# Kernel optimization log

Measured on AMD Instinct MI355X. Metric: run time of the kernel, lower is better.

Reference implementation:

```python
import jax, jax.numpy as jnp
import numpy as np

N = 20000      # nodes
E = 640000     # edges (avg degree 32)
IN = 32        # input_dim
HID = 256      # hidden_dim
H = 8          # num_heads
Dh = HID // H  # head_dim = 32
TD = 32        # time_dim
L = 3          # num_layers
OUT = 2


def setup_inputs() -> dict:
    key = jax.random.key(0)
    ks = jax.random.split(key, 20)
    def w(k, sh):
        return (jax.random.normal(k, sh, jnp.float32) * 0.05)
    return {
        "x": jax.random.normal(ks[0], (N, IN), jnp.float32),
        "timestamps": jax.random.uniform(ks[1], (N,), jnp.float32),
        "edge_index": jax.random.randint(ks[2], (2, E), 0, N, jnp.int32),
        "batch": jnp.zeros((N,), jnp.int32),
        "time_freq": jax.random.normal(ks[3], (TD // 2,), jnp.float32),
        "inW": w(ks[4], (IN, HID)), "inb": jnp.zeros((HID,), jnp.float32),
        "qW": w(ks[5], (L, HID + TD, HID)), "qb": jnp.zeros((L, HID), jnp.float32),
        "kW": w(ks[6], (L, HID + TD, HID)), "kb": jnp.zeros((L, HID), jnp.float32),
        "vW": w(ks[7], (L, HID, HID)), "vb": jnp.zeros((L, HID), jnp.float32),
        "oW": w(ks[8], (L, HID, HID)), "ob": jnp.zeros((L, HID), jnp.float32),
        "c1W": w(ks[9], (HID, HID // 2)), "c1b": jnp.zeros((HID // 2,), jnp.float32),
        "c2W": w(ks[10], (HID // 2, OUT)), "c2b": jnp.zeros((OUT,), jnp.float32),
    }


def reference(x, timestamps, time_freq, inW, inb, qW, qb, kW, kb, vW, vb,
              oW, ob, c1W, c1b, c2W, c2b, edge_index, batch):
    n = x.shape[0]
    src, dst = edge_index[0], edge_index[1]

    # Functional time encoding (node-level timestamps branch)
    t = (timestamps - timestamps.min()) / (timestamps.max() - timestamps.min() + 1e-8)
    wt = t[:, None] * time_freq[None, :]                      # [N, TD/2]
    tf = jnp.concatenate([jnp.cos(wt), jnp.sin(wt)], axis=-1)  # [N, TD]

    h = x @ inW + inb                                          # [N, HID]
    scale = 1.0 / np.sqrt(Dh).astype(np.float32)

    for l in range(L):
        xt = jnp.concatenate([h, tf], axis=-1)                 # [N, HID+TD]
        Q = (xt @ qW[l] + qb[l]).reshape(n, H, Dh)
        K = (xt @ kW[l] + kb[l]).reshape(n, H, Dh)
        V = (h @ vW[l] + vb[l]).reshape(n, H, Dh)

        # per-edge attention scores [E, H]
        scores = jnp.einsum('ehd,ehd->eh', Q[dst], K[src]) * scale

        # segment softmax over incoming edges of each dst node
        m = jax.ops.segment_max(scores, dst, num_segments=n)   # [N, H]
        e = jnp.exp(scores - m[dst])
        s = jax.ops.segment_sum(e, dst, num_segments=n)        # [N, H]
        att = e / s[dst]                                       # [E, H]

        msgs = att[..., None] * V[src]                         # [E, H, Dh]
        out = jax.ops.segment_sum(msgs, dst, num_segments=n)   # [N, H, Dh]
        out = out.reshape(n, HID) @ oW[l] + ob[l]
        h = jax.nn.elu(out)

    # global mean pool (single graph: batch all zeros)
    cnt = jax.ops.segment_sum(jnp.ones((n, 1), h.dtype), batch, num_segments=1)
    g = jax.ops.segment_sum(h, batch, num_segments=1) / jnp.maximum(cnt, 1.0)

    logits = jax.nn.relu(g @ c1W + c1b) @ c2W + c2b            # [1, OUT]
    return logits
```

## Files before the change

### kernel.cpp

```cpp
#include <hip/hip_runtime.h>
#include <math.h>

#define HID 256
#define TD 32
#define NL 3
#define C1DIM 128
#define OUTDIM 2
#define QKVW 768

using half8  = __attribute__((ext_vector_type(8))) _Float16;
using half4v = __attribute__((ext_vector_type(4))) _Float16;
using half2v = __attribute__((ext_vector_type(2))) _Float16;
using f32x4  = __attribute__((ext_vector_type(4))) float;

typedef __attribute__((address_space(1))) void gbl_void_t;
typedef __attribute__((address_space(3))) void lds_void_t;

__device__ __forceinline__ void load16_to_lds(const void* g, void* l) {
  __builtin_amdgcn_global_load_lds((const gbl_void_t*)g, (lds_void_t*)l, 16, 0, 0);
}

__device__ __forceinline__ float dot8h(half8 a, half8 b, float acc) {
#if __has_builtin(__builtin_amdgcn_fdot2)
  union { half8 v; half2v h2[4]; } ua, ub;
  ua.v = a; ub.v = b;
#pragma unroll
  for (int j = 0; j < 4; ++j) acc = __builtin_amdgcn_fdot2(ua.h2[j], ub.h2[j], acc, false);
  return acc;
#else
#pragma unroll
  for (int j = 0; j < 8; ++j) acc += (float)a[j] * (float)b[j];
  return acc;
#endif
}

__global__ __launch_bounds__(1024) void k_tsmm(const float* __restrict__ ts,
                                               float* __restrict__ mmf,
                                               int* __restrict__ deg, int n) {
  int t = threadIdx.x;
  float lmin = INFINITY, lmax = -INFINITY;
  for (int i = t; i < n; i += 1024) {
    float v = ts[i];
    lmin = fminf(lmin, v);
    lmax = fmaxf(lmax, v);
    deg[i] = 0;
  }
#pragma unroll
  for (int off = 32; off >= 1; off >>= 1) {
    lmin = fminf(lmin, __shfl_xor(lmin, off));
    lmax = fmaxf(lmax, __shfl_xor(lmax, off));
  }
  __shared__ float wmin[16], wmax[16];
  int lane = t & 63, w = t >> 6;
  if (lane == 0) { wmin[w] = lmin; wmax[w] = lmax; }
  __syncthreads();
  if (t == 0) {
    float a = INFINITY, b = -INFINITY;
    for (int i = 0; i < 16; ++i) { a = fminf(a, wmin[i]); b = fmaxf(b, wmax[i]); }
    mmf[0] = a; mmf[1] = b;
  }
}

__global__ void k_enc(const float* __restrict__ ts, const float* __restrict__ freq,
                      const float* __restrict__ mmf, const float* __restrict__ x,
                      _Float16* __restrict__ tfh, _Float16* __restrict__ xh, int n) {
  int idx = blockIdx.x * blockDim.x + threadIdx.x;
  int nt = n * TD;
  if (idx < nt) {
    int node = idx >> 5, j = idx & 31;
    float t = (ts[node] - mmf[0]) / (mmf[1] - mmf[0] + 1e-8f);
    float w = t * freq[j & 15];
    tfh[idx] = (_Float16)((j < 16) ? cosf(w) : sinf(w));
  } else if (idx < nt + n * 32) {
    int i2 = idx - nt;
    xh[i2] = (_Float16)x[i2];
  }
}

__global__ void k_prep(const float* __restrict__ inW, const float* __restrict__ qW,
                       const float* __restrict__ kW, const float* __restrict__ vW,
                       const float* __restrict__ oW, const float* __restrict__ qb,
                       const float* __restrict__ kb, const float* __restrict__ vb,
                       _Float16* __restrict__ inWt, _Float16* __restrict__ qkvWt,
                       float* __restrict__ qkvb, _Float16* __restrict__ oWt) {
  int idx = blockIdx.x * blockDim.x + threadIdx.x;
  const int S0 = 32 * HID;
  const int KQ = HID + TD;
  const int S1 = NL * QKVW * KQ;
  const int S2 = NL * QKVW;
  const int S3 = NL * HID * HID;
  if (idx < S0) {
    int nrow = idx / 32, k = idx - nrow * 32;
    inWt[idx] = (_Float16)inW[k * HID + nrow];
  } else if ((idx -= S0) < S1) {
    int l = idx / (QKVW * KQ);
    int rem = idx - l * (QKVW * KQ);
    int nrow = rem / KQ;
    int k = rem - nrow * KQ;
    float v;
    if (nrow < 256)      v = qW[(size_t)l * KQ * HID + (size_t)k * HID + nrow];
    else if (nrow < 512) v = kW[(size_t)l * KQ * HID + (size_t)k * HID + (nrow - 256)];
    else                 v = (k < HID) ? vW[(size_t)l * HID * HID + (size_t)k * HID + (nrow - 512)] : 0.f;
    qkvWt[idx] = (_Float16)v;
  } else if ((idx -= S1) < S2) {
    int l = idx / QKVW;
    int j = idx - l * QKVW;
    float v;
    if (j < 256)      v = qb[l * HID + j];
    else if (j < 512) v = kb[l * HID + (j - 256)];
    else              v = vb[l * HID + (j - 512)];
    qkvb[idx] = v;
  } else if ((idx -= S2) < S3) {
    int l = idx / (HID * HID);
    int rem = idx - l * (HID * HID);
    int nrow = rem / HID;
    int k = rem - nrow * HID;
    oWt[idx] = (_Float16)oW[(size_t)l * HID * HID + (size_t)k * HID + nrow];
  }
}

__global__ void k_count(const int* __restrict__ dst, int* deg, int e) {
  int i = blockIdx.x * blockDim.x + threadIdx.x;
  if (i < e) atomicAdd(&deg[dst[i]], 1);
}

__global__ __launch_bounds__(256) void k_scan_part(const int* __restrict__ deg,
                                                   int* __restrict__ bsum, int n) {
  int t = threadIdx.x;
  int idx = blockIdx.x * 256 + t;
  int v = (idx < n) ? deg[idx] : 0;
  int lane = t & 63, w = t >> 6;
  int x = v;
#pragma unroll
  for (int off = 1; off < 64; off <<= 1) {
    int y = __shfl_up(x, off);
    if (lane >= off) x += y;
  }
  __shared__ int ws[4];
  if (lane == 63) ws[w] = x;
  __syncthreads();
  if (t == 0) bsum[blockIdx.x] = ws[0] + ws[1] + ws[2] + ws[3];
}

__global__ __launch_bounds__(64) void k_scan_mid(const int* __restrict__ bsum,
                                                 int* __restrict__ boff, int nb) {
  int lane = threadIdx.x;
  int carry = 0;
  for (int base = 0; base < nb; base += 64) {
    int i = base + lane;
    int v = (i < nb) ? bsum[i] : 0;
    int x = v;
#pragma unroll
    for (int off = 1; off < 64; off <<= 1) {
      int y = __shfl_up(x, off);
      if (lane >= off) x += y;
    }
    if (i < nb) boff[i] = carry + x - v;
    carry += __shfl(x, 63);
  }
}

__global__ __launch_bounds__(256) void k_scan_apply(const int* __restrict__ deg,
                                                    const int* __restrict__ boff,
                                                    int* __restrict__ row_ptr,
                                                    int* __restrict__ cursor, int n, int e) {
  int t = threadIdx.x;
  int idx = blockIdx.x * 256 + t;
  int v = (idx < n) ? deg[idx] : 0;
  int lane = t & 63, w = t >> 6;
  int x = v;
#pragma unroll
  for (int off = 1; off < 64; off <<= 1) {
    int y = __shfl_up(x, off);
    if (lane >= off) x += y;
  }
  __shared__ int ws[4];
  if (lane == 63) ws[w] = x;
  __syncthreads();
  int wpre = 0;
  for (int i = 0; i < w; ++i) wpre += ws[i];
  if (idx < n) {
    row_ptr[idx] = boff[blockIdx.x] + wpre + x - v;
    cursor[idx] = 0;
  }
  if (idx == 0) row_ptr[n] = e;
}

__global__ void k_scatter(const int* __restrict__ src, const int* __restrict__ dst,
                          const int* __restrict__ row_ptr, int* cursor,
                          int* __restrict__ colbuf, int e) {
  int i = blockIdx.x * blockDim.x + threadIdx.x;
  if (i >= e) return;
  int d = dst[i];
  int p = atomicAdd(&cursor[d], 1);
  colbuf[row_ptr[d] + p] = src[i];
}

__global__ __launch_bounds__(256) void k_gemm_f16(
    const _Float16* __restrict__ A1, int K1,
    const _Float16* __restrict__ A2, int K2,
    const _Float16* __restrict__ Bt,
    const float* __restrict__ bias,
    _Float16* __restrict__ C,
    _Float16* __restrict__ Qb,
    _Float16* __restrict__ KV,
    int M, int Ncols, int Ktot, int mode) {
  __shared__ half8 smem8[2 * 768];
  char* smem = (char*)smem8;
  const int tid = threadIdx.x;
  const int lane = tid & 63, wave = tid >> 6;
  const int wm = wave >> 1, wn = wave & 1;
  const int row0 = blockIdx.y * 128;
  const int col0 = blockIdx.x * 64;

  auto stage = [&](int buf, int k0) {
    char* sA = smem + buf * 12288;
    char* sB = sA + 8192;
#pragma unroll
    for (int i = 0; i < 2; ++i) {
      int kg = i * 2 + (wave >> 1);
      int row = (wave & 1) * 64 + lane;
      int grow = row0 + row; if (grow > M - 1) grow = M - 1;
      int k = k0 + kg * 8;
      const _Float16* src = (k < K1) ? (A1 + (size_t)grow * K1 + k)
                                     : (A2 + (size_t)grow * K2 + (k - K1));
      load16_to_lds(src, sA + (i * 256 + wave * 64) * 16);
    }
    {
      const _Float16* src = Bt + (size_t)(col0 + lane) * Ktot + k0 + wave * 8;
      load16_to_lds(src, sB + wave * 64 * 16);
    }
  };

  f32x4 acc[4][2];
#pragma unroll
  for (int mf = 0; mf < 4; ++mf)
#pragma unroll
    for (int nf = 0; nf < 2; ++nf) acc[mf][nf] = f32x4{0.f, 0.f, 0.f, 0.f};

  const int nsteps = Ktot >> 5;
  int cur = 0;
  stage(0, 0);
  __syncthreads();
  for (int st = 0; st < nsteps; ++st) {
    if (st + 1 < nsteps) stage(cur ^ 1, (st + 1) * 32);
    char* sA = smem + cur * 12288;
    char* sB = sA + 8192;
    half8 af[4], bf[2];
#pragma unroll
    for (int mf = 0; mf < 4; ++mf) {
      int slot = (lane >> 4) * 128 + wm * 64 + mf * 16 + (lane & 15);
      af[mf] = *(const half8*)(sA + slot * 16);
    }
#pragma unroll
    for (int nf = 0; nf < 2; ++nf) {
      int slot = (lane >> 4) * 64 + wn * 32 + nf * 16 + (lane & 15);
      bf[nf] = *(const half8*)(sB + slot * 16);
    }
#pragma unroll
    for (int mf = 0; mf < 4; ++mf)
#pragma unroll
      for (int nf = 0; nf < 2; ++nf)
        acc[mf][nf] = __builtin_amdgcn_mfma_f32_16x16x32_f16(af[mf], bf[nf], acc[mf][nf], 0, 0, 0);
    __syncthreads();
    cur ^= 1;
  }

  const int rbase = row0 + wm * 64 + (lane >> 4) * 4;
  const int cbase = col0 + wn * 32 + (lane & 15);
#pragma unroll
  for (int nf = 0; nf < 2; ++nf) {
    int col = cbase + nf * 16;
    float bv = bias[col];
    if (mode != 2) {
#pragma unroll
      for (int mf = 0; mf < 4; ++mf) {
#pragma unroll
        for (int r = 0; r < 4; ++r) {
          int row = rbase + mf * 16 + r;
          if (row < M) {
            float v = acc[mf][nf][r] + bv;
            if (mode == 1) v = (v > 0.f) ? v : expm1f(v);
            C[(size_t)row * Ncols + col] = (_Float16)v;
          }
        }
      }
    } else {
      bool isQ = col < 256;
      int cc = col - 256;
      int isV = cc >> 8;
      int c2 = cc & 255;
      int hh = c2 >> 5, dim = c2 & 31;
      size_t kvoff = ((size_t)hh * M) * 64 + isV * 32 + dim;
#pragma unroll
      for (int mf = 0; mf < 4; ++mf) {
#pragma unroll
        for (int r = 0; r < 4; ++r) {
          int row = rbase + mf * 16 + r;
          if (row < M) {
            float v = acc[mf][nf][r] + bv;
            if (isQ) Qb[(size_t)row * HID + col] = (_Float16)v;
            else     KV[kvoff + (size_t)row * 64] = (_Float16)v;
          }
        }
      }
    }
  }
}

__global__ __launch_bounds__(256) void k_attn(const _Float16* __restrict__ Qb,
                                              const _Float16* __restrict__ KV,
                                              const int* __restrict__ row_ptr,
                                              const int* __restrict__ colbuf,
                                              _Float16* __restrict__ out, int n) {
  int h = blockIdx.x & 7;
  int node = (blockIdx.x >> 3) * 64 + (threadIdx.x >> 2);
  if (node >= n) return;
  int j = threadIdx.x & 3;
  const float scale = 0.17677669529663687f;
  const _Float16* KVh = KV + ((size_t)h * n) * 64;

  half8 qh = *(const half8*)(Qb + (size_t)node * HID + h * 32 + j * 8);
  half8 qs;
#pragma unroll
  for (int q = 0; q < 8; ++q) qs[q] = (_Float16)((float)qh[q] * scale);

  int beg = row_ptr[node], end = row_ptr[node + 1];
  float m = -INFINITY, s = 0.f;
  float a[8] = {0.f, 0.f, 0.f, 0.f, 0.f, 0.f, 0.f, 0.f};

  for (int i = beg; i < end; i += 4) {
    half8 kk[4], vv[4];
#pragma unroll
    for (int t = 0; t < 4; ++t) {
      int ii = i + t; if (ii > end - 1) ii = end - 1;
      int sn = colbuf[ii];
      const _Float16* b = KVh + ((size_t)sn) * 64 + j * 8;
      kk[t] = *(const half8*)(b);
      vv[t] = *(const half8*)(b + 32);
    }
    float p[4];
#pragma unroll
    for (int t = 0; t < 4; ++t) p[t] = dot8h(qs, kk[t], 0.f);
#pragma unroll
    for (int t = 0; t < 4; ++t) {
      p[t] += __shfl_xor(p[t], 1);
      p[t] += __shfl_xor(p[t], 2);
      if (i + t >= end) p[t] = -INFINITY;
    }
#pragma unroll
    for (int t = 0; t < 4; ++t) {
      float sc_ = p[t];
      if (sc_ <= m) {
        float e2 = __expf(sc_ - m);
        s += e2;
#pragma unroll
        for (int q = 0; q < 8; ++q) a[q] = fmaf(e2, (float)vv[t][q], a[q]);
      } else {
        float f = __expf(m - sc_);
        s = s * f + 1.f;
#pragma unroll
        for (int q = 0; q < 8; ++q) a[q] = fmaf(a[q], f, (float)vv[t][q]);
        m = sc_;
      }
    }
  }

  float inv = (s > 0.f) ? (1.f / s) : 0.f;
  half8 o;
#pragma unroll
  for (int q = 0; q < 8; ++q) o[q] = (_Float16)(a[q] * inv);
  *(half8*)(out + (size_t)node * HID + h * 32 + j * 8) = o;
}

__global__ __launch_bounds__(256) void k_pool_partial(const _Float16* __restrict__ h,
                                                      float* __restrict__ partial, int n) {
  int b = blockIdx.x, t = threadIdx.x;
  float s = 0.f;
  for (int r = b; r < n; r += 256) s += (float)h[(size_t)r * HID + t];
  partial[b * HID + t] = s;
}

__global__ __launch_bounds__(256) void k_final(const float* __restrict__ partial,
                                               const float* __restrict__ c1W,
                                               const float* __restrict__ c1b,
                                               const float* __restrict__ c2W,
                                               const float* __restrict__ c2b,
                                               float* __restrict__ out, int n) {
  __shared__ float gl[HID];
  __shared__ float r1[C1DIM];
  int t = threadIdx.x;
  float s = 0.f;
  for (int b = 0; b < 256; b++) s += partial[b * HID + t];
  gl[t] = s / (float)n;
  __syncthreads();
  if (t < C1DIM) {
    float a = c1b[t];
    for (int k = 0; k < HID; k++) a += gl[k] * c1W[k * C1DIM + t];
    r1[t] = fmaxf(a, 0.f);
  }
  __syncthreads();
  if (t < OUTDIM) {
    float a = c2b[t];
    for (int k = 0; k < C1DIM; k++) a += r1[k] * c2W[k * OUTDIM + t];
    out[t] = a;
  }
}

extern "C" void kernel_launch(void* const* d_in, const int* in_sizes, int n_in,
                              void* d_out, int out_size, void* d_ws, size_t ws_size,
                              hipStream_t stream) {
  const float* x    = (const float*)d_in[0];
  const float* ts   = (const float*)d_in[1];
  const int*   ei   = (const int*)d_in[2];
  const float* freq = (const float*)d_in[4];
  const float* inW  = (const float*)d_in[5];
  const float* inb  = (const float*)d_in[6];
  const float* qW   = (const float*)d_in[7];
  const float* qb   = (const float*)d_in[8];
  const float* kW   = (const float*)d_in[9];
  const float* kb   = (const float*)d_in[10];
  const float* vW   = (const float*)d_in[11];
  const float* vb   = (const float*)d_in[12];
  const float* oW   = (const float*)d_in[13];
  const float* ob   = (const float*)d_in[14];
  const float* c1W  = (const float*)d_in[15];
  const float* c1b  = (const float*)d_in[16];
  const float* c2W  = (const float*)d_in[17];
  const float* c2b  = (const float*)d_in[18];

  int n = in_sizes[1];
  int e = in_sizes[2] / 2;
  const int* src = ei;
  const int* dst = ei + e;
  int nb = (n + 255) / 256;

  char* w = (char*)d_ws;
  size_t off = 0;
  auto alloc = [&](size_t bytes) -> char* {
    char* p = w + off;
    off = (off + bytes + 255) & ~(size_t)255;
    return p;
  };
  _Float16* tfh     = (_Float16*)alloc((size_t)n * TD * 2);
  _Float16* xh      = (_Float16*)alloc((size_t)n * 32 * 2);
  _Float16* h       = (_Float16*)alloc((size_t)n * HID * 2);
  _Float16* Qbuf    = (_Float16*)alloc((size_t)n * HID * 2);
  _Float16* KV      = (_Float16*)alloc((size_t)n * 512 * 2);
  _Float16* ao      = (_Float16*)alloc((size_t)n * HID * 2);
  _Float16* inWt    = (_Float16*)alloc((size_t)32 * HID * 2);
  _Float16* qkvWt   = (_Float16*)alloc((size_t)NL * QKVW * (HID + TD) * 2);
  float*    qkvb    = (float*)alloc((size_t)NL * QKVW * 4);
  _Float16* oWt     = (_Float16*)alloc((size_t)NL * HID * HID * 2);
  int*      deg     = (int*)alloc((size_t)n * 4);
  int*      cursor  = (int*)alloc((size_t)n * 4);
  int*      row_ptr = (int*)alloc((size_t)(n + 1) * 4);
  int*      colbuf  = (int*)alloc((size_t)e * 4);
  int*      bsum    = (int*)alloc((size_t)nb * 4);
  int*      boff    = (int*)alloc((size_t)nb * 4);
  float*    partial = (float*)alloc((size_t)256 * HID * 4);
  float*    mmf     = (float*)alloc(256);

  int b256 = 256;
  hipLaunchKernelGGL(k_tsmm, dim3(1), dim3(1024), 0, stream, ts, mmf, deg, n);
  hipLaunchKernelGGL(k_enc, dim3((n * 64 + 255) / 256), dim3(b256), 0, stream,
                     ts, freq, mmf, x, tfh, xh, n);
  {
    int total = 32 * HID + NL * QKVW * (HID + TD) + NL * QKVW + NL * HID * HID;
    hipLaunchKernelGGL(k_prep, dim3((total + 255) / 256), dim3(b256), 0, stream,
                       inW, qW, kW, vW, oW, qb, kb, vb, inWt, qkvWt, qkvb, oWt);
  }
  hipLaunchKernelGGL(k_count, dim3((e + 255) / 256), dim3(b256), 0, stream, dst, deg, e);
  hipLaunchKernelGGL(k_scan_part, dim3(nb), dim3(b256), 0, stream, deg, bsum, n);
  hipLaunchKernelGGL(k_scan_mid, dim3(1), dim3(64), 0, stream, bsum, boff, nb);
  hipLaunchKernelGGL(k_scan_apply, dim3(nb), dim3(b256), 0, stream, deg, boff, row_ptr, cursor, n, e);
  hipLaunchKernelGGL(k_scatter, dim3((e + 255) / 256), dim3(b256), 0, stream, src, dst, row_ptr, cursor, colbuf, e);

  dim3 ggrid_h(HID / 64, (n + 127) / 128);
  dim3 ggrid_qkv(QKVW / 64, (n + 127) / 128);
  hipLaunchKernelGGL(k_gemm_f16, ggrid_h, dim3(b256), 0, stream,
                     xh, 32, xh, 32, inWt, inb, h, (_Float16*)nullptr, (_Float16*)nullptr,
                     n, HID, 32, 0);

  int nchunks = (n + 63) / 64;
  for (int l = 0; l < NL; ++l) {
    const _Float16* qkvWtl = qkvWt + (size_t)l * QKVW * (HID + TD);
    const float*    qkvbl  = qkvb + (size_t)l * QKVW;
    const _Float16* oWtl   = oWt + (size_t)l * HID * HID;
    hipLaunchKernelGGL(k_gemm_f16, ggrid_qkv, dim3(b256), 0, stream,
                       h, HID, tfh, TD, qkvWtl, qkvbl, (_Float16*)nullptr, Qbuf, KV,
                       n, QKVW, HID + TD, 2);
    hipLaunchKernelGGL(k_attn, dim3(nchunks * 8), dim3(b256), 0, stream,
                       Qbuf, KV, row_ptr, colbuf, ao, n);
    hipLaunchKernelGGL(k_gemm_f16, ggrid_h, dim3(b256), 0, stream,
                       ao, HID, ao, HID, oWtl, ob + l * HID, h, (_Float16*)nullptr, (_Float16*)nullptr,
                       n, HID, HID, 1);
  }

  hipLaunchKernelGGL(k_pool_partial, dim3(256), dim3(b256), 0, stream, h, partial, n);
  hipLaunchKernelGGL(k_final, dim3(1), dim3(b256), 0, stream, partial, c1W, c1b, c2W, c2b, (float*)d_out, n);
}
```

Baseline: 481.1 us.

## Fuse setup kernels and widen QKV GEMM tile to 128x128

```diff
diff --git a/kernel.cpp b/kernel.cpp
--- a/kernel.cpp
+++ b/kernel.cpp
@@ -9,7 +9,6 @@
 #define QKVW 768
 
 using half8  = __attribute__((ext_vector_type(8))) _Float16;
-using half4v = __attribute__((ext_vector_type(4))) _Float16;
 using half2v = __attribute__((ext_vector_type(2))) _Float16;
 using f32x4  = __attribute__((ext_vector_type(4))) float;
 
@@ -34,88 +33,147 @@
 #endif
 }
 
-__global__ __launch_bounds__(1024) void k_tsmm(const float* __restrict__ ts,
-                                               float* __restrict__ mmf,
-                                               int* __restrict__ deg, int n) {
+#define NB_ENC 512
+#define NB_QKV (NL * 9 * 12)
+#define NB_O   (NL * 8 * 4)
+#define NB_IN  4
+#define NB_B   9
+
+__global__ __launch_bounds__(256) void k_setup(
+    const float* __restrict__ ts, const float* __restrict__ freq,
+    const float* __restrict__ x,
+    const float* __restrict__ inW, const float* __restrict__ qW,
+    const float* __restrict__ kW, const float* __restrict__ vW,
+    const float* __restrict__ oW, const float* __restrict__ qb,
+    const float* __restrict__ kb, const float* __restrict__ vb,
+    _Float16* __restrict__ tfh, _Float16* __restrict__ xh,
+    _Float16* __restrict__ inWt, _Float16* __restrict__ qkvWt,
+    float* __restrict__ qkvb, _Float16* __restrict__ oWt, int n) {
+  __shared__ _Float16 lds[32][65];
+  int bid = blockIdx.x;
   int t = threadIdx.x;
-  float lmin = INFINITY, lmax = -INFINITY;
-  for (int i = t; i < n; i += 1024) {
-    float v = ts[i];
-    lmin = fminf(lmin, v);
-    lmax = fmaxf(lmax, v);
-    deg[i] = 0;
-  }
-#pragma unroll
-  for (int off = 32; off >= 1; off >>= 1) {
-    lmin = fminf(lmin, __shfl_xor(lmin, off));
-    lmax = fmaxf(lmax, __shfl_xor(lmax, off));
-  }
-  __shared__ float wmin[16], wmax[16];
-  int lane = t & 63, w = t >> 6;
-  if (lane == 0) { wmin[w] = lmin; wmax[w] = lmax; }
-  __syncthreads();
-  if (t == 0) {
-    float a = INFINITY, b = -INFINITY;
-    for (int i = 0; i < 16; ++i) { a = fminf(a, wmin[i]); b = fmaxf(b, wmax[i]); }
-    mmf[0] = a; mmf[1] = b;
-  }
-}
-
-__global__ void k_enc(const float* __restrict__ ts, const float* __restrict__ freq,
-                      const float* __restrict__ mmf, const float* __restrict__ x,
-                      _Float16* __restrict__ tfh, _Float16* __restrict__ xh, int n) {
-  int idx = blockIdx.x * blockDim.x + threadIdx.x;
-  int nt = n * TD;
-  if (idx < nt) {
-    int node = idx >> 5, j = idx & 31;
-    float t = (ts[node] - mmf[0]) / (mmf[1] - mmf[0] + 1e-8f);
-    float w = t * freq[j & 15];
-    tfh[idx] = (_Float16)((j < 16) ? cosf(w) : sinf(w));
-  } else if (idx < nt + n * 32) {
-    int i2 = idx - nt;
-    xh[i2] = (_Float16)x[i2];
-  }
-}
-
-__global__ void k_prep(const float* __restrict__ inW, const float* __restrict__ qW,
-                       const float* __restrict__ kW, const float* __restrict__ vW,
-                       const float* __restrict__ oW, const float* __restrict__ qb,
-                       const float* __restrict__ kb, const float* __restrict__ vb,
-                       _Float16* __restrict__ inWt, _Float16* __restrict__ qkvWt,
-                       float* __restrict__ qkvb, _Float16* __restrict__ oWt) {
-  int idx = blockIdx.x * blockDim.x + threadIdx.x;
-  const int S0 = 32 * HID;
   const int KQ = HID + TD;
-  const int S1 = NL * QKVW * KQ;
-  const int S2 = NL * QKVW;
-  const int S3 = NL * HID * HID;
-  if (idx < S0) {
-    int nrow = idx / 32, k = idx - nrow * 32;
-    inWt[idx] = (_Float16)inW[k * HID + nrow];
-  } else if ((idx -= S0) < S1) {
-    int l = idx / (QKVW * KQ);
-    int rem = idx - l * (QKVW * KQ);
-    int nrow = rem / KQ;
-    int k = rem - nrow * KQ;
-    float v;
-    if (nrow < 256)      v = qW[(size_t)l * KQ * HID + (size_t)k * HID + nrow];
-    else if (nrow < 512) v = kW[(size_t)l * KQ * HID + (size_t)k * HID + (nrow - 256)];
-    else                 v = (k < HID) ? vW[(size_t)l * HID * HID + (size_t)k * HID + (nrow - 512)] : 0.f;
-    qkvWt[idx] = (_Float16)v;
-  } else if ((idx -= S1) < S2) {
-    int l = idx / QKVW;
-    int j = idx - l * QKVW;
-    float v;
-    if (j < 256)      v = qb[l * HID + j];
-    else if (j < 512) v = kb[l * HID + (j - 256)];
-    else              v = vb[l * HID + (j - 512)];
-    qkvb[idx] = v;
-  } else if ((idx -= S2) < S3) {
-    int l = idx / (HID * HID);
-    int rem = idx - l * (HID * HID);
-    int nrow = rem / HID;
-    int k = rem - nrow * HID;
-    oWt[idx] = (_Float16)oW[(size_t)l * HID * HID + (size_t)k * HID + nrow];
+
+  if (bid < NB_ENC) {
+    float lmin = INFINITY, lmax = -INFINITY;
+    for (int i = t; i < n; i += 256) {
+      float v = ts[i];
+      lmin = fminf(lmin, v); lmax = fmaxf(lmax, v);
+    }
+#pragma unroll
+    for (int off = 32; off >= 1; off >>= 1) {
+      lmin = fminf(lmin, __shfl_xor(lmin, off));
+      lmax = fmaxf(lmax, __shfl_xor(lmax, off));
+    }
+    __shared__ float wmin[4], wmax[4];
+    int lane = t & 63, w = t >> 6;
+    if (lane == 0) { wmin[w] = lmin; wmax[w] = lmax; }
+    __syncthreads();
+    float tmin = fminf(fminf(wmin[0], wmin[1]), fminf(wmin[2], wmin[3]));
+    float tmax = fmaxf(fmaxf(wmax[0], wmax[1]), fmaxf(wmax[2], wmax[3]));
+    float inv = 1.f / (tmax - tmin + 1e-8f);
+    int nt = n * TD;
+    int total = n * 64;
+    for (int idx = bid * 256 + t; idx < total; idx += NB_ENC * 256) {
+      if (idx < nt) {
+        int node = idx >> 5, j = idx & 31;
+        float tv = (ts[node] - tmin) * inv;
+        float wv = tv * freq[j & 15];
+        tfh[idx] = (_Float16)((j < 16) ? cosf(wv) : sinf(wv));
+      } else {
+        int i2 = idx - nt;
+        xh[i2] = (_Float16)x[i2];
+      }
+    }
+    return;
+  }
+  bid -= NB_ENC;
+
+  if (bid < NB_QKV) {
+    int l = bid / 108;
+    int rem = bid - l * 108;
+    int kt = rem / 12, ntile = rem - kt * 12;
+    int k0 = kt * 32, n0 = ntile * 64;
+#pragma unroll
+    for (int it = 0; it < 8; ++it) {
+      int i = it * 256 + t;
+      int kk = i >> 6, nn = i & 63;
+      int k = k0 + kk, nrow = n0 + nn;
+      float v;
+      if (nrow < 256)      v = qW[(size_t)l * KQ * HID + (size_t)k * HID + nrow];
+      else if (nrow < 512) v = kW[(size_t)l * KQ * HID + (size_t)k * HID + (nrow - 256)];
+      else                 v = (k < HID) ? vW[(size_t)l * HID * HID + (size_t)k * HID + (nrow - 512)] : 0.f;
+      lds[kk][nn] = (_Float16)v;
+    }
+    __syncthreads();
+    {
+      int nn = t >> 2, kq = (t & 3) * 8;
+      _Float16* dst = qkvWt + (size_t)l * QKVW * KQ + (size_t)(n0 + nn) * KQ + k0 + kq;
+      half8 v;
+#pragma unroll
+      for (int j = 0; j < 8; ++j) v[j] = lds[kq + j][nn];
+      *(half8*)dst = v;
+    }
+    return;
+  }
+  bid -= NB_QKV;
+
+  if (bid < NB_O) {
+    int l = bid / 32;
+    int rem = bid - l * 32;
+    int kt = rem / 4, ntile = rem - kt * 4;
+    int k0 = kt * 32, n0 = ntile * 64;
+#pragma unroll
+    for (int it = 0; it < 8; ++it) {
+      int i = it * 256 + t;
+      int kk = i >> 6, nn = i & 63;
+      lds[kk][nn] = (_Float16)oW[(size_t)l * HID * HID + (size_t)(k0 + kk) * HID + n0 + nn];
+    }
+    __syncthreads();
+    {
+      int nn = t >> 2, kq = (t & 3) * 8;
+      _Float16* dst = oWt + (size_t)l * HID * HID + (size_t)(n0 + nn) * HID + k0 + kq;
+      half8 v;
+#pragma unroll
+      for (int j = 0; j < 8; ++j) v[j] = lds[kq + j][nn];
+      *(half8*)dst = v;
+    }
+    return;
+  }
+  bid -= NB_O;
+
+  if (bid < NB_IN) {
+    int n0 = bid * 64;
+#pragma unroll
+    for (int it = 0; it < 8; ++it) {
+      int i = it * 256 + t;
+      int kk = i >> 6, nn = i & 63;
+      lds[kk][nn] = (_Float16)inW[(size_t)kk * HID + n0 + nn];
+    }
+    __syncthreads();
+    {
+      int nn = t >> 2, kq = (t & 3) * 8;
+      _Float16* dst = inWt + (size_t)(n0 + nn) * 32 + kq;
+      half8 v;
+#pragma unroll
+      for (int j = 0; j < 8; ++j) v[j] = lds[kq + j][nn];
+      *(half8*)dst = v;
+    }
+    return;
+  }
+  bid -= NB_IN;
+
+  {
+    int idx = bid * 256 + t;
+    if (idx < NL * QKVW) {
+      int l = idx / QKVW;
+      int j = idx - l * QKVW;
+      float v;
+      if (j < 256)      v = qb[l * HID + j];
+      else if (j < 512) v = kb[l * HID + (j - 256)];
+      else              v = vb[l * HID + (j - 512)];
+      qkvb[idx] = v;
+    }
   }
 }
 
@@ -202,8 +260,6 @@
     const _Float16* __restrict__ Bt,
     const float* __restrict__ bias,
     _Float16* __restrict__ C,
-    _Float16* __restrict__ Qb,
-    _Float16* __restrict__ KV,
     int M, int Ncols, int Ktot, int mode) {
   __shared__ half8 smem8[2 * 768];
   char* smem = (char*)smem8;
@@ -272,36 +328,112 @@
   for (int nf = 0; nf < 2; ++nf) {
     int col = cbase + nf * 16;
     float bv = bias[col];
-    if (mode != 2) {
-#pragma unroll
-      for (int mf = 0; mf < 4; ++mf) {
-#pragma unroll
-        for (int r = 0; r < 4; ++r) {
-          int row = rbase + mf * 16 + r;
-          if (row < M) {
-            float v = acc[mf][nf][r] + bv;
-            if (mode == 1) v = (v > 0.f) ? v : expm1f(v);
-            C[(size_t)row * Ncols + col] = (_Float16)v;
-          }
+#pragma unroll
+    for (int mf = 0; mf < 4; ++mf) {
+#pragma unroll
+      for (int r = 0; r < 4; ++r) {
+        int row = rbase + mf * 16 + r;
+        if (row < M) {
+          float v = acc[mf][nf][r] + bv;
+          if (mode == 1) v = (v > 0.f) ? v : expm1f(v);
+          C[(size_t)row * Ncols + col] = (_Float16)v;
         }
       }
-    } else {
-      bool isQ = col < 256;
-      int cc = col - 256;
-      int isV = cc >> 8;
-      int c2 = cc & 255;
-      int hh = c2 >> 5, dim = c2 & 31;
-      size_t kvoff = ((size_t)hh * M) * 64 + isV * 32 + dim;
-#pragma unroll
-      for (int mf = 0; mf < 4; ++mf) {
-#pragma unroll
-        for (int r = 0; r < 4; ++r) {
-          int row = rbase + mf * 16 + r;
-          if (row < M) {
-            float v = acc[mf][nf][r] + bv;
-            if (isQ) Qb[(size_t)row * HID + col] = (_Float16)v;
-            else     KV[kvoff + (size_t)row * 64] = (_Float16)v;
-          }
+    }
+  }
+}
+
+__global__ __launch_bounds__(256) void k_gemm_qkv(
+    const _Float16* __restrict__ A1, int K1,
+    const _Float16* __restrict__ A2, int K2,
+    const _Float16* __restrict__ Bt,
+    const float* __restrict__ bias,
+    _Float16* __restrict__ Qb,
+    _Float16* __restrict__ KV,
+    int M, int Ktot) {
+  __shared__ half8 smem8[2048];
+  char* smem = (char*)smem8;
+  const int tid = threadIdx.x;
+  const int lane = tid & 63, wave = tid >> 6;
+  const int wm = wave >> 1, wn = wave & 1;
+  const int row0 = blockIdx.y * 128;
+  const int col0 = blockIdx.x * 128;
+
+  auto stage = [&](int buf, int k0) {
+    char* sA = smem + buf * 16384;
+    char* sB = sA + 8192;
+    int k = k0 + wave * 8;
+#pragma unroll
+    for (int j = 0; j < 2; ++j) {
+      int row = j * 64 + lane;
+      int grow = row0 + row; if (grow > M - 1) grow = M - 1;
+      const _Float16* srcA = (k < K1) ? (A1 + (size_t)grow * K1 + k)
+                                      : (A2 + (size_t)grow * K2 + (k - K1));
+      load16_to_lds(srcA, sA + (wave * 128 + j * 64) * 16);
+    }
+#pragma unroll
+    for (int j = 0; j < 2; ++j) {
+      int col = j * 64 + lane;
+      const _Float16* srcB = Bt + (size_t)(col0 + col) * Ktot + k;
+      load16_to_lds(srcB, sB + (wave * 128 + j * 64) * 16);
+    }
+  };
+
+  f32x4 acc[4][4];
+#pragma unroll
+  for (int mf = 0; mf < 4; ++mf)
+#pragma unroll
+    for (int nf = 0; nf < 4; ++nf) acc[mf][nf] = f32x4{0.f, 0.f, 0.f, 0.f};
+
+  const int nsteps = Ktot >> 5;
+  int cur = 0;
+  stage(0, 0);
+  __syncthreads();
+  for (int st = 0; st < nsteps; ++st) {
+    if (st + 1 < nsteps) stage(cur ^ 1, (st + 1) * 32);
+    char* sA = smem + cur * 16384;
+    char* sB = sA + 8192;
+    half8 af[4], bf[4];
+#pragma unroll
+    for (int mf = 0; mf < 4; ++mf) {
+      int slot = (lane >> 4) * 128 + wm * 64 + mf * 16 + (lane & 15);
+      af[mf] = *(const half8*)(sA + slot * 16);
+    }
+#pragma unroll
+    for (int nf = 0; nf < 4; ++nf) {
+      int slot = (lane >> 4) * 128 + wn * 64 + nf * 16 + (lane & 15);
+      bf[nf] = *(const half8*)(sB + slot * 16);
+    }
+#pragma unroll
+    for (int mf = 0; mf < 4; ++mf)
+#pragma unroll
+      for (int nf = 0; nf < 4; ++nf)
+        acc[mf][nf] = __builtin_amdgcn_mfma_f32_16x16x32_f16(af[mf], bf[nf], acc[mf][nf], 0, 0, 0);
+    __syncthreads();
+    cur ^= 1;
+  }
+
+  const int rbase = row0 + wm * 64 + (lane >> 4) * 4;
+  const int cbase = col0 + wn * 64 + (lane & 15);
+#pragma unroll
+  for (int nf = 0; nf < 4; ++nf) {
+    int col = cbase + nf * 16;
+    float bv = bias[col];
+    bool isQ = col < 256;
+    int cc = col - 256;
+    int isV = cc >> 8;
+    int c2 = cc & 255;
+    int hh = c2 >> 5, dim = c2 & 31;
+    size_t kvoff = ((size_t)hh * M) * 64 + isV * 32 + dim;
+#pragma unroll
+    for (int mf = 0; mf < 4; ++mf) {
+#pragma unroll
+      for (int r = 0; r < 4; ++r) {
+        int row = rbase + mf * 16 + r;
+        if (row < M) {
+          float v = acc[mf][nf][r] + bv;
+          if (isQ) Qb[(size_t)row * HID + col] = (_Float16)v;
+          else     KV[kvoff + (size_t)row * 64] = (_Float16)v;
         }
       }
     }
@@ -459,16 +591,14 @@
   int*      bsum    = (int*)alloc((size_t)nb * 4);
   int*      boff    = (int*)alloc((size_t)nb * 4);
   float*    partial = (float*)alloc((size_t)256 * HID * 4);
-  float*    mmf     = (float*)alloc(256);
 
   int b256 = 256;
-  hipLaunchKernelGGL(k_tsmm, dim3(1), dim3(1024), 0, stream, ts, mmf, deg, n);
-  hipLaunchKernelGGL(k_enc, dim3((n * 64 + 255) / 256), dim3(b256), 0, stream,
-                     ts, freq, mmf, x, tfh, xh, n);
+  hipMemsetAsync(deg, 0, (size_t)n * 4, stream);
   {
-    int total = 32 * HID + NL * QKVW * (HID + TD) + NL * QKVW + NL * HID * HID;
-    hipLaunchKernelGGL(k_prep, dim3((total + 255) / 256), dim3(b256), 0, stream,
-                       inW, qW, kW, vW, oW, qb, kb, vb, inWt, qkvWt, qkvb, oWt);
+    int nblk = NB_ENC + NB_QKV + NB_O + NB_IN + NB_B;
+    hipLaunchKernelGGL(k_setup, dim3(nblk), dim3(b256), 0, stream,
+                       ts, freq, x, inW, qW, kW, vW, oW, qb, kb, vb,
+                       tfh, xh, inWt, qkvWt, qkvb, oWt, n);
   }
   hipLaunchKernelGGL(k_count, dim3((e + 255) / 256), dim3(b256), 0, stream, dst, deg, e);
   hipLaunchKernelGGL(k_scan_part, dim3(nb), dim3(b256), 0, stream, deg, bsum, n);
@@ -477,24 +607,21 @@
   hipLaunchKernelGGL(k_scatter, dim3((e + 255) / 256), dim3(b256), 0, stream, src, dst, row_ptr, cursor, colbuf, e);
 
   dim3 ggrid_h(HID / 64, (n + 127) / 128);
-  dim3 ggrid_qkv(QKVW / 64, (n + 127) / 128);
+  dim3 ggrid_qkv(QKVW / 128, (n + 127) / 128);
   hipLaunchKernelGGL(k_gemm_f16, ggrid_h, dim3(b256), 0, stream,
-                     xh, 32, xh, 32, inWt, inb, h, (_Float16*)nullptr, (_Float16*)nullptr,
-                     n, HID, 32, 0);
+                     xh, 32, xh, 32, inWt, inb, h, n, HID, 32, 0);
 
   int nchunks = (n + 63) / 64;
   for (int l = 0; l < NL; ++l) {
     const _Float16* qkvWtl = qkvWt + (size_t)l * QKVW * (HID + TD);
     const float*    qkvbl  = qkvb + (size_t)l * QKVW;
     const _Float16* oWtl   = oWt + (size_t)l * HID * HID;
-    hipLaunchKernelGGL(k_gemm_f16, ggrid_qkv, dim3(b256), 0, stream,
-                       h, HID, tfh, TD, qkvWtl, qkvbl, (_Float16*)nullptr, Qbuf, KV,
-                       n, QKVW, HID + TD, 2);
+    hipLaunchKernelGGL(k_gemm_qkv, ggrid_qkv, dim3(b256), 0, stream,
+                       h, HID, tfh, TD, qkvWtl, qkvbl, Qbuf, KV, n, HID + TD);
     hipLaunchKernelGGL(k_attn, dim3(nchunks * 8), dim3(b256), 0, stream,
                        Qbuf, KV, row_ptr, colbuf, ao, n);
     hipLaunchKernelGGL(k_gemm_f16, ggrid_h, dim3(b256), 0, stream,
-                       ao, HID, ao, HID, oWtl, ob + l * HID, h, (_Float16*)nullptr, (_Float16*)nullptr,
-                       n, HID, HID, 1);
+                       ao, HID, ao, HID, oWtl, ob + l * HID, h, n, HID, HID, 1);
   }
 
   hipLaunchKernelGGL(k_pool_partial, dim3(256), dim3(b256), 0, stream, h, partial, n);
```

New measurement: 493.5 us. 2.6% more time.
